# Optimization experiments

Hardware: AMD Instinct MI355X
Metric: run time of the kernel (lower is better)

## Reference

```python
import jax, jax.numpy as jnp
import numpy as np

N_NODES = 100000
N_EDGES = 1280000
IN_CH = 64
OUT_CH = 64


def setup_inputs() -> dict:
    key = jax.random.key(0)
    k1, k2, k3, k4 = jax.random.split(key, 4)
    x = jax.random.normal(k1, (N_NODES, IN_CH), dtype=jnp.float32)
    edge_index = jax.random.randint(k2, (2, N_EDGES), 0, N_NODES, dtype=jnp.int64)
    # GraphConv params (glorot weight, zero bias)
    scale = jnp.sqrt(6.0 / (IN_CH + OUT_CH)).astype(jnp.float32)
    W = jax.random.uniform(k3, (IN_CH, OUT_CH), dtype=jnp.float32, minval=-scale, maxval=scale)
    b = jnp.zeros((OUT_CH,), dtype=jnp.float32)
    return {"x": x, "edge_index": edge_index, "W": W, "b": b}


def reference(x, edge_index, W, b):
    # DGL GraphConv, norm='both': out = D_in^{-1/2} A^T (D_out^{-1/2} x W) + b
    src, dst = edge_index[0], edge_index[1]
    ones = jnp.ones((src.shape[0],), dtype=x.dtype)
    out_deg = jax.ops.segment_sum(ones, src, num_segments=N_NODES)
    in_deg = jax.ops.segment_sum(ones, dst, num_segments=N_NODES)
    norm_src = jnp.where(out_deg > 0, jax.lax.rsqrt(jnp.maximum(out_deg, 1.0)), 0.0)
    norm_dst = jnp.where(in_deg > 0, jax.lax.rsqrt(jnp.maximum(in_deg, 1.0)), 0.0)
    # in_feats <= out_feats: transform first, then aggregate
    h = (x * norm_src[:, None]) @ W              # [N, OUT_CH]
    msg = h[src]                                 # gather  [E, OUT_CH]
    agg = jax.ops.segment_sum(msg, dst, num_segments=N_NODES)  # scatter-add [N, OUT_CH]
    return agg * norm_dst[:, None] + b
```

## Files before the change

kernel.cpp:

```cpp
#include <hip/hip_runtime.h>
#include <hip/hip_fp16.h>

#define CH 64
#define CAP 32
#define SPILLMAX 4096
#define RANGE 12500
#define SLICES 64
#define TILE 2048
#define EPT 8
#define BSH 9
#define BKT 512

__global__ __launch_bounds__(256) void histA_kernel(const int* __restrict__ src,
                                                    const int* __restrict__ dst,
                                                    unsigned short* __restrict__ partial,
                                                    int* __restrict__ tileHist,
                                                    int* __restrict__ nspill,
                                                    int E, int N, int R, int NT)
{
    __shared__ int h[RANGE];
    int tid = threadIdx.x;
    int bid = blockIdx.x;
    if (bid < NT) {
        if (bid == 0 && tid == 0) nspill[0] = 0;
        h[tid] = 0;
        __syncthreads();
        int e0 = bid * TILE + tid * EPT;
        if (e0 + EPT <= E) {
            const int4* dp = (const int4*)(dst + e0);
            int4 a = dp[0], b = dp[1];
            atomicAdd(&h[a.x >> BSH], 1); atomicAdd(&h[a.y >> BSH], 1);
            atomicAdd(&h[a.z >> BSH], 1); atomicAdd(&h[a.w >> BSH], 1);
            atomicAdd(&h[b.x >> BSH], 1); atomicAdd(&h[b.y >> BSH], 1);
            atomicAdd(&h[b.z >> BSH], 1); atomicAdd(&h[b.w >> BSH], 1);
        } else {
            for (int k = e0; k < E && k < e0 + EPT; ++k) atomicAdd(&h[dst[k] >> BSH], 1);
        }
        __syncthreads();
        tileHist[bid * 256 + tid] = h[tid];
    } else {
        int hb = bid - NT;
        int r  = hb % R;
        int sl = hb / R;
        int lo = r * RANGE;
        int hi = min(lo + RANGE, N);
        int span = hi - lo;
        for (int i = tid; i < span; i += 256) h[i] = 0;
        __syncthreads();
        int per = (E + SLICES - 1) / SLICES;
        int sb = sl * per, se = min(sb + per, E);
        for (int e = sb + tid * 4; e < se; e += 256 * 4) {
            if (e + 4 <= se) {
                int4 v = *(const int4*)(src + e);
                if (v.x >= lo && v.x < hi) atomicAdd(&h[v.x - lo], 1);
                if (v.y >= lo && v.y < hi) atomicAdd(&h[v.y - lo], 1);
                if (v.z >= lo && v.z < hi) atomicAdd(&h[v.z - lo], 1);
                if (v.w >= lo && v.w < hi) atomicAdd(&h[v.w - lo], 1);
            } else {
                for (int k = e; k < se; ++k) {
                    int sv = src[k];
                    if (sv >= lo && sv < hi) atomicAdd(&h[sv - lo], 1);
                }
            }
        }
        __syncthreads();
        unsigned short* pp = partial + (size_t)hb * RANGE;
        for (int i = tid; i < span; i += 256) pp[i] = (unsigned short)h[i];
    }
}

__global__ __launch_bounds__(256) void rpscaleB_kernel(const unsigned short* __restrict__ partial,
                                                       const float* __restrict__ x,
                                                       __half* __restrict__ xh,
                                                       int* __restrict__ tileHist,
                                                       int* __restrict__ totals,
                                                       int N, int R, int NT, int NPB)
{
    __shared__ float nsl[256];
    __shared__ int sm[256];
    int tid = threadIdx.x;
    int bid = blockIdx.x;
    if (bid < NPB) {
        int n0 = bid * 256;
        int n = n0 + tid;
        if (n < N) {
            int r = n / RANGE, off = n - r * RANGE;
            int s = 0;
            #pragma unroll 8
            for (int sl = 0; sl < SLICES; ++sl)
                s += partial[(size_t)(sl * R + r) * RANGE + off];
            nsl[tid] = (s > 0) ? rsqrtf((float)s) : 0.0f;
        } else {
            nsl[tid] = 0.0f;
        }
        __syncthreads();
        int sub = tid & 7;
        int nl0 = tid >> 3;
        for (int p = 0; p < 8; ++p) {
            int nl = p * 32 + nl0;
            int node = n0 + nl;
            if (node >= N) break;
            float ns = nsl[nl];
            const float4* xp = (const float4*)(x + (size_t)node * CH + sub * 8);
            float4 a = xp[0], b = xp[1];
            __half2 h0 = __floats2half2_rn(a.x * ns, a.y * ns);
            __half2 h1 = __floats2half2_rn(a.z * ns, a.w * ns);
            __half2 h2 = __floats2half2_rn(b.x * ns, b.y * ns);
            __half2 h3 = __floats2half2_rn(b.z * ns, b.w * ns);
            uint4 u;
            u.x = (unsigned)__half_as_ushort(h0.x) | ((unsigned)__half_as_ushort(h0.y) << 16);
            u.y = (unsigned)__half_as_ushort(h1.x) | ((unsigned)__half_as_ushort(h1.y) << 16);
            u.z = (unsigned)__half_as_ushort(h2.x) | ((unsigned)__half_as_ushort(h2.y) << 16);
            u.w = (unsigned)__half_as_ushort(h3.x) | ((unsigned)__half_as_ushort(h3.y) << 16);
            *(uint4*)(xh + (size_t)node * CH + sub * 8) = u;
        }
    } else {
        int b = bid - NPB;
        int C = (NT + 255) / 256;
        int vals[8];
        int s = 0;
        for (int k = 0; k < C; ++k) {
            int t = tid * C + k;
            vals[k] = (t < NT) ? tileHist[t * 256 + b] : 0;
            s += vals[k];
        }
        sm[tid] = s;
        __syncthreads();
        for (int d = 1; d < 256; d <<= 1) {
            int v = (tid >= d) ? sm[tid - d] : 0;
            __syncthreads();
            sm[tid] += v;
            __syncthreads();
        }
        int off = (tid > 0) ? sm[tid - 1] : 0;
        for (int k = 0; k < C; ++k) {
            int t = tid * C + k;
            if (t < NT) { tileHist[t * 256 + b] = off; off += vals[k]; }
        }
        if (tid == 255) totals[b] = sm[255];
    }
}

__global__ __launch_bounds__(256) void binC_kernel(const int* __restrict__ src,
                                                   const int* __restrict__ dst,
                                                   const int* __restrict__ tileBase,
                                                   const int* __restrict__ totals,
                                                   int* __restrict__ sorted, int E, int NB)
{
    __shared__ int sm[256];
    __shared__ int gb[256];
    __shared__ int lcnt[256];
    __shared__ int lbase[256];
    __shared__ int slotVal[TILE];
    int tid = threadIdx.x;
    int t = blockIdx.x;
    sm[tid] = (tid < NB) ? totals[tid] : 0;
    lcnt[tid] = 0;
    __syncthreads();
    for (int d = 1; d < 256; d <<= 1) {
        int v = (tid >= d) ? sm[tid - d] : 0;
        __syncthreads();
        sm[tid] += v;
        __syncthreads();
    }
    int bb = (tid > 0) ? sm[tid - 1] : 0;
    gb[tid] = (tid < NB) ? bb + tileBase[t * 256 + tid] : 0;
    __syncthreads();
    int e0 = t * TILE + tid * EPT;
    int s[EPT], d[EPT], rk[EPT], pb[EPT];
    int nk = 0;
    if (e0 + EPT <= E) {
        const int4* sp = (const int4*)(src + e0);
        const int4* dp = (const int4*)(dst + e0);
        int4 a = sp[0], b = sp[1], c = dp[0], f = dp[1];
        s[0]=a.x; s[1]=a.y; s[2]=a.z; s[3]=a.w; s[4]=b.x; s[5]=b.y; s[6]=b.z; s[7]=b.w;
        d[0]=c.x; d[1]=c.y; d[2]=c.z; d[3]=c.w; d[4]=f.x; d[5]=f.y; d[6]=f.z; d[7]=f.w;
        nk = EPT;
    } else {
        for (int k = 0; e0 + k < E && k < EPT; ++k) { s[k] = src[e0+k]; d[k] = dst[e0+k]; nk++; }
    }
    for (int k = 0; k < nk; ++k) {
        pb[k] = d[k] >> BSH;
        rk[k] = atomicAdd(&lcnt[pb[k]], 1);
    }
    __syncthreads();
    sm[tid] = lcnt[tid];
    __syncthreads();
    for (int dd = 1; dd < 256; dd <<= 1) {
        int v = (tid >= dd) ? sm[tid - dd] : 0;
        __syncthreads();
        sm[tid] += v;
        __syncthreads();
    }
    lbase[tid] = (tid > 0) ? sm[tid - 1] : 0;
    int total = sm[255];
    __syncthreads();
    for (int k = 0; k < nk; ++k)
        slotVal[lbase[pb[k]] + rk[k]] = (s[k] << BSH) | (d[k] & (BKT - 1));
    __syncthreads();
    for (int i = tid; i < total; i += 256) {
        int lo = 0, hi = 255;
        #pragma unroll
        for (int st = 0; st < 8; ++st) {
            int mid = (lo + hi + 1) >> 1;
            if (lbase[mid] <= i) lo = mid; else hi = mid - 1;
        }
        sorted[gb[lo] + (i - lbase[lo])] = slotVal[i];
    }
}

__global__ __launch_bounds__(256) void binD_kernel(const int* __restrict__ sorted,
                                                   const int* __restrict__ totals,
                                                   int* __restrict__ bucket,
                                                   int* __restrict__ cnt,
                                                   int* __restrict__ spill,
                                                   int* __restrict__ nspill, int N, int NB)
{
    __shared__ int sm[256];
    __shared__ int lc[BKT];
    int b = blockIdx.x, tid = threadIdx.x;
    sm[tid] = (tid < NB) ? totals[tid] : 0;
    lc[tid] = 0; lc[tid + 256] = 0;
    __syncthreads();
    for (int d = 1; d < 256; d <<= 1) {
        int v = (tid >= d) ? sm[tid - d] : 0;
        __syncthreads();
        sm[tid] += v;
        __syncthreads();
    }
    int beg = (b > 0) ? sm[b - 1] : 0;
    int end = sm[b];
    int nbase = b << BSH;
    for (int i = beg + tid; i < end; i += 256) {
        int v = sorted[i];
        int sv = v >> BSH;
        int dl = v & (BKT - 1);
        int pos = atomicAdd(&lc[dl], 1);
        if (pos < CAP) {
            bucket[(size_t)(nbase + dl) * CAP + pos] = sv;
        } else {
            int sp = atomicAdd(nspill, 1);
            if (sp < SPILLMAX) { spill[2*sp] = nbase + dl; spill[2*sp+1] = sv; }
        }
    }
    __syncthreads();
    int n0 = nbase + tid;
    if (n0 < N) cnt[n0] = lc[tid];
    int n1 = nbase + 256 + tid;
    if (n1 < N) cnt[n1] = lc[256 + tid];
}

__global__ __launch_bounds__(256) void agg_kernel(const __half* __restrict__ xh,
                                                  const int* __restrict__ bucket,
                                                  const int* __restrict__ cnt,
                                                  const int* __restrict__ spill,
                                                  const int* __restrict__ nspill,
                                                  __half* __restrict__ aggh, int N)
{
    int hw0 = (blockIdx.x * blockDim.x + threadIdx.x) >> 5;
    int nHW = (gridDim.x * blockDim.x) >> 5;
    int sl = threadIdx.x & 31;
    for (int node = hw0; node < N; node += nHW) {
        int c = cnt[node];
        int m = (c < CAP) ? c : CAP;
        const int* bp = bucket + (size_t)node * CAP;
        float ax0 = 0, ay0 = 0, ax1 = 0, ay1 = 0, ax2 = 0, ay2 = 0, ax3 = 0, ay3 = 0;
        int j = 0;
        for (; j + 8 <= m; j += 8) {
            int4 va = *(const int4*)(bp + j);
            int4 vb = *(const int4*)(bp + j + 4);
            float2 f0 = __half22float2(*(const __half2*)(xh + (size_t)va.x * CH + sl * 2));
            float2 f1 = __half22float2(*(const __half2*)(xh + (size_t)va.y * CH + sl * 2));
            float2 f2 = __half22float2(*(const __half2*)(xh + (size_t)va.z * CH + sl * 2));
            float2 f3 = __half22float2(*(const __half2*)(xh + (size_t)va.w * CH + sl * 2));
            float2 f4 = __half22float2(*(const __half2*)(xh + (size_t)vb.x * CH + sl * 2));
            float2 f5 = __half22float2(*(const __half2*)(xh + (size_t)vb.y * CH + sl * 2));
            float2 f6 = __half22float2(*(const __half2*)(xh + (size_t)vb.z * CH + sl * 2));
            float2 f7 = __half22float2(*(const __half2*)(xh + (size_t)vb.w * CH + sl * 2));
            ax0 += f0.x + f4.x; ay0 += f0.y + f4.y;
            ax1 += f1.x + f5.x; ay1 += f1.y + f5.y;
            ax2 += f2.x + f6.x; ay2 += f2.y + f6.y;
            ax3 += f3.x + f7.x; ay3 += f3.y + f7.y;
        }
        for (; j + 4 <= m; j += 4) {
            int4 va = *(const int4*)(bp + j);
            float2 f0 = __half22float2(*(const __half2*)(xh + (size_t)va.x * CH + sl * 2));
            float2 f1 = __half22float2(*(const __half2*)(xh + (size_t)va.y * CH + sl * 2));
            float2 f2 = __half22float2(*(const __half2*)(xh + (size_t)va.z * CH + sl * 2));
            float2 f3 = __half22float2(*(const __half2*)(xh + (size_t)va.w * CH + sl * 2));
            ax0 += f0.x; ay0 += f0.y;
            ax1 += f1.x; ay1 += f1.y;
            ax2 += f2.x; ay2 += f2.y;
            ax3 += f3.x; ay3 += f3.y;
        }
        for (; j < m; ++j) {
            float2 f = __half22float2(*(const __half2*)(xh + (size_t)bp[j] * CH + sl * 2));
            ax0 += f.x; ay0 += f.y;
        }
        if (c > CAP) {
            int ns = *nspill;
            if (ns > SPILLMAX) ns = SPILLMAX;
            for (int i = 0; i < ns; ++i) {
                if (spill[2 * i] == node) {
                    float2 f = __half22float2(*(const __half2*)(xh + (size_t)spill[2 * i + 1] * CH + sl * 2));
                    ax0 += f.x; ay0 += f.y;
                }
            }
        }
        float nd = (c > 0) ? rsqrtf((float)c) : 0.0f;
        float rx = ((ax0 + ax1) + (ax2 + ax3)) * nd;
        float ry = ((ay0 + ay1) + (ay2 + ay3)) * nd;
        *(__half2*)(aggh + (size_t)node * CH + sl * 2) = __floats2half2_rn(rx, ry);
    }
}

__global__ __launch_bounds__(256) void gemm_out_kernel(const __half* __restrict__ aggh,
                                                       const float* __restrict__ W,
                                                       const float* __restrict__ bias,
                                                       float* __restrict__ out, int N)
{
    int g = blockIdx.x * 256 + threadIdx.x;
    int waveId = __builtin_amdgcn_readfirstlane(g >> 6);
    int lane = threadIdx.x & 63;
    int quarter = waveId & 3;
    int row = ((waveId >> 2) << 6) + lane;
    if (row >= N) return;
    const int cbase = quarter * 16;
    float acc[16];
    #pragma unroll
    for (int i = 0; i < 16; ++i) acc[i] = 0.0f;
    const __half* xp = aggh + (size_t)row * CH;
    for (int k0 = 0; k0 < CH; k0 += 8) {
        uint4 u = *(const uint4*)(xp + k0);
        const __half2* hp = (const __half2*)&u;
        float xk[8];
        #pragma unroll
        for (int j = 0; j < 4; ++j) {
            float2 f = __half22float2(hp[j]);
            xk[2 * j] = f.x; xk[2 * j + 1] = f.y;
        }
        #pragma unroll
        for (int kk = 0; kk < 8; ++kk) {
            const float* wrow = W + (k0 + kk) * CH + cbase;
            #pragma unroll
            for (int q = 0; q < 4; ++q) {
                float4 w = *(const float4*)(wrow + q * 4);
                acc[q * 4 + 0] += xk[kk] * w.x;
                acc[q * 4 + 1] += xk[kk] * w.y;
                acc[q * 4 + 2] += xk[kk] * w.z;
                acc[q * 4 + 3] += xk[kk] * w.w;
            }
        }
    }
    float* op = out + (size_t)row * CH + cbase;
    #pragma unroll
    for (int q = 0; q < 4; ++q) {
        float4 b = *(const float4*)(bias + cbase + q * 4);
        float4 o;
        o.x = acc[q * 4 + 0] + b.x;
        o.y = acc[q * 4 + 1] + b.y;
        o.z = acc[q * 4 + 2] + b.z;
        o.w = acc[q * 4 + 3] + b.w;
        *(float4*)(op + q * 4) = o;
    }
}

extern "C" void kernel_launch(void* const* d_in, const int* in_sizes, int n_in,
                              void* d_out, int out_size, void* d_ws, size_t ws_size,
                              hipStream_t stream)
{
    const float* x    = (const float*)d_in[0];
    const int*   edge = (const int*)d_in[1];
    const float* W    = (const float*)d_in[2];
    const float* bias = (const float*)d_in[3];
    float* out = (float*)d_out;

    int N = in_sizes[0] / CH;
    int E = in_sizes[1] / 2;
    const int* src = edge;
    const int* dst = edge + E;
    int R   = (N + RANGE - 1) / RANGE;
    int NT  = (E + TILE - 1) / TILE;
    int NB  = (N + BKT - 1) >> BSH;
    int NPB = (N + 255) / 256;

    int* nspill  = (int*)d_ws;
    int* spill   = nspill + 64;
    int* cnt     = spill + 2 * SPILLMAX;
    int* bucket  = cnt + N;
    unsigned short* partial = (unsigned short*)(bucket + (size_t)N * CAP);
    int* tileHist = (int*)(partial + (size_t)SLICES * R * RANGE);
    int* totals   = tileHist + NT * 256;
    int* sorted   = (int*)partial;
    size_t endoff = (char*)(totals + 320) - (char*)d_ws;
    size_t xoff = (endoff + 255) & ~(size_t)255;
    __half* xh = (__half*)((char*)d_ws + xoff);
    size_t aoff = ((xoff + (size_t)N * CH * sizeof(__half)) + 255) & ~(size_t)255;
    __half* aggh = (__half*)((char*)d_ws + aoff);

    histA_kernel<<<NT + R * SLICES, 256, 0, stream>>>(src, dst, partial, tileHist,
                                                      nspill, E, N, R, NT);
    rpscaleB_kernel<<<NPB + NB, 256, 0, stream>>>(partial, x, xh, tileHist, totals,
                                                  N, R, NT, NPB);
    binC_kernel<<<NT, 256, 0, stream>>>(src, dst, tileHist, totals, sorted, E, NB);
    binD_kernel<<<NB, 256, 0, stream>>>(sorted, totals, bucket, cnt, spill, nspill, N, NB);
    agg_kernel<<<4096, 256, 0, stream>>>(xh, bucket, cnt, spill, nspill, aggh, N);
    int nwaves = 4 * ((N + 63) / 64);
    gemm_out_kernel<<<(nwaves + 3) / 4, 256, 0, stream>>>(aggh, W, bias, out, N);
}
```

Baseline: 109.0 us.

## Pack out-degree histogram into 16-bit LDS counters and flatten agg grid

The out-degree histogram now packs two 16-bit counters per 32-bit LDS word, so each block covers 25000 nodes instead of 12500. That halves the range count R, while SLICES doubles to 128 to keep the block count. This halves the redundant source scans per slice, at the cost of shift/mask work and a reduction over twice as many partials in rpscaleB. The aggregation kernel also drops its grid-stride loop and launches one half-wave per node. Packed counters could overflow if a node got more than 65535 hits in one slice.

```diff
diff --git a/kernel.cpp b/kernel.cpp
--- a/kernel.cpp
+++ b/kernel.cpp
@@ -4,8 +4,9 @@
 #define CH 64
 #define CAP 32
 #define SPILLMAX 4096
-#define RANGE 12500
-#define SLICES 64
+#define HBINS 12500
+#define HSPAN 25000
+#define SLICES 128
 #define TILE 2048
 #define EPT 8
 #define BSH 9
@@ -13,12 +14,12 @@
 
 __global__ __launch_bounds__(256) void histA_kernel(const int* __restrict__ src,
                                                     const int* __restrict__ dst,
-                                                    unsigned short* __restrict__ partial,
+                                                    int* __restrict__ partial,
                                                     int* __restrict__ tileHist,
                                                     int* __restrict__ nspill,
                                                     int E, int N, int R, int NT)
 {
-    __shared__ int h[RANGE];
+    __shared__ int h[HBINS];
     int tid = threadIdx.x;
     int bid = blockIdx.x;
     if (bid < NT) {
@@ -42,34 +43,33 @@
         int hb = bid - NT;
         int r  = hb % R;
         int sl = hb / R;
-        int lo = r * RANGE;
-        int hi = min(lo + RANGE, N);
-        int span = hi - lo;
-        for (int i = tid; i < span; i += 256) h[i] = 0;
+        int lo = r * HSPAN;
+        int hi = min(lo + HSPAN, N);
+        for (int i = tid; i < HBINS; i += 256) h[i] = 0;
         __syncthreads();
         int per = (E + SLICES - 1) / SLICES;
         int sb = sl * per, se = min(sb + per, E);
         for (int e = sb + tid * 4; e < se; e += 256 * 4) {
             if (e + 4 <= se) {
                 int4 v = *(const int4*)(src + e);
-                if (v.x >= lo && v.x < hi) atomicAdd(&h[v.x - lo], 1);
-                if (v.y >= lo && v.y < hi) atomicAdd(&h[v.y - lo], 1);
-                if (v.z >= lo && v.z < hi) atomicAdd(&h[v.z - lo], 1);
-                if (v.w >= lo && v.w < hi) atomicAdd(&h[v.w - lo], 1);
+                if (v.x >= lo && v.x < hi) { int i0 = v.x - lo; atomicAdd(&h[i0 >> 1], 1u << ((i0 & 1) << 4)); }
+                if (v.y >= lo && v.y < hi) { int i1 = v.y - lo; atomicAdd(&h[i1 >> 1], 1u << ((i1 & 1) << 4)); }
+                if (v.z >= lo && v.z < hi) { int i2 = v.z - lo; atomicAdd(&h[i2 >> 1], 1u << ((i2 & 1) << 4)); }
+                if (v.w >= lo && v.w < hi) { int i3 = v.w - lo; atomicAdd(&h[i3 >> 1], 1u << ((i3 & 1) << 4)); }
             } else {
                 for (int k = e; k < se; ++k) {
                     int sv = src[k];
-                    if (sv >= lo && sv < hi) atomicAdd(&h[sv - lo], 1);
+                    if (sv >= lo && sv < hi) { int ii = sv - lo; atomicAdd(&h[ii >> 1], 1u << ((ii & 1) << 4)); }
                 }
             }
         }
         __syncthreads();
-        unsigned short* pp = partial + (size_t)hb * RANGE;
-        for (int i = tid; i < span; i += 256) pp[i] = (unsigned short)h[i];
-    }
-}
-
-__global__ __launch_bounds__(256) void rpscaleB_kernel(const unsigned short* __restrict__ partial,
+        int* pp = partial + (size_t)hb * HBINS;
+        for (int i = tid; i < HBINS; i += 256) pp[i] = h[i];
+    }
+}
+
+__global__ __launch_bounds__(256) void rpscaleB_kernel(const int* __restrict__ partial,
                                                        const float* __restrict__ x,
                                                        __half* __restrict__ xh,
                                                        int* __restrict__ tileHist,
@@ -84,11 +84,14 @@
         int n0 = bid * 256;
         int n = n0 + tid;
         if (n < N) {
-            int r = n / RANGE, off = n - r * RANGE;
+            int r = n / HSPAN;
+            int idx = n - r * HSPAN;
+            int word = idx >> 1;
+            int sh = (idx & 1) << 4;
             int s = 0;
             #pragma unroll 8
             for (int sl = 0; sl < SLICES; ++sl)
-                s += partial[(size_t)(sl * R + r) * RANGE + off];
+                s += (partial[(size_t)(sl * R + r) * HBINS + word] >> sh) & 0xFFFF;
             nsl[tid] = (s > 0) ? rsqrtf((float)s) : 0.0f;
         } else {
             nsl[tid] = 0.0f;
@@ -257,61 +260,59 @@
                                                   const int* __restrict__ nspill,
                                                   __half* __restrict__ aggh, int N)
 {
-    int hw0 = (blockIdx.x * blockDim.x + threadIdx.x) >> 5;
-    int nHW = (gridDim.x * blockDim.x) >> 5;
+    int node = (blockIdx.x * blockDim.x + threadIdx.x) >> 5;
     int sl = threadIdx.x & 31;
-    for (int node = hw0; node < N; node += nHW) {
-        int c = cnt[node];
-        int m = (c < CAP) ? c : CAP;
-        const int* bp = bucket + (size_t)node * CAP;
-        float ax0 = 0, ay0 = 0, ax1 = 0, ay1 = 0, ax2 = 0, ay2 = 0, ax3 = 0, ay3 = 0;
-        int j = 0;
-        for (; j + 8 <= m; j += 8) {
-            int4 va = *(const int4*)(bp + j);
-            int4 vb = *(const int4*)(bp + j + 4);
-            float2 f0 = __half22float2(*(const __half2*)(xh + (size_t)va.x * CH + sl * 2));
-            float2 f1 = __half22float2(*(const __half2*)(xh + (size_t)va.y * CH + sl * 2));
-            float2 f2 = __half22float2(*(const __half2*)(xh + (size_t)va.z * CH + sl * 2));
-            float2 f3 = __half22float2(*(const __half2*)(xh + (size_t)va.w * CH + sl * 2));
-            float2 f4 = __half22float2(*(const __half2*)(xh + (size_t)vb.x * CH + sl * 2));
-            float2 f5 = __half22float2(*(const __half2*)(xh + (size_t)vb.y * CH + sl * 2));
-            float2 f6 = __half22float2(*(const __half2*)(xh + (size_t)vb.z * CH + sl * 2));
-            float2 f7 = __half22float2(*(const __half2*)(xh + (size_t)vb.w * CH + sl * 2));
-            ax0 += f0.x + f4.x; ay0 += f0.y + f4.y;
-            ax1 += f1.x + f5.x; ay1 += f1.y + f5.y;
-            ax2 += f2.x + f6.x; ay2 += f2.y + f6.y;
-            ax3 += f3.x + f7.x; ay3 += f3.y + f7.y;
-        }
-        for (; j + 4 <= m; j += 4) {
-            int4 va = *(const int4*)(bp + j);
-            float2 f0 = __half22float2(*(const __half2*)(xh + (size_t)va.x * CH + sl * 2));
-            float2 f1 = __half22float2(*(const __half2*)(xh + (size_t)va.y * CH + sl * 2));
-            float2 f2 = __half22float2(*(const __half2*)(xh + (size_t)va.z * CH + sl * 2));
-            float2 f3 = __half22float2(*(const __half2*)(xh + (size_t)va.w * CH + sl * 2));
-            ax0 += f0.x; ay0 += f0.y;
-            ax1 += f1.x; ay1 += f1.y;
-            ax2 += f2.x; ay2 += f2.y;
-            ax3 += f3.x; ay3 += f3.y;
-        }
-        for (; j < m; ++j) {
-            float2 f = __half22float2(*(const __half2*)(xh + (size_t)bp[j] * CH + sl * 2));
-            ax0 += f.x; ay0 += f.y;
-        }
-        if (c > CAP) {
-            int ns = *nspill;
-            if (ns > SPILLMAX) ns = SPILLMAX;
-            for (int i = 0; i < ns; ++i) {
-                if (spill[2 * i] == node) {
-                    float2 f = __half22float2(*(const __half2*)(xh + (size_t)spill[2 * i + 1] * CH + sl * 2));
-                    ax0 += f.x; ay0 += f.y;
-                }
+    if (node >= N) return;
+    int c = cnt[node];
+    int m = (c < CAP) ? c : CAP;
+    const int* bp = bucket + (size_t)node * CAP;
+    float ax0 = 0, ay0 = 0, ax1 = 0, ay1 = 0, ax2 = 0, ay2 = 0, ax3 = 0, ay3 = 0;
+    int j = 0;
+    for (; j + 8 <= m; j += 8) {
+        int4 va = *(const int4*)(bp + j);
+        int4 vb = *(const int4*)(bp + j + 4);
+        float2 f0 = __half22float2(*(const __half2*)(xh + (size_t)va.x * CH + sl * 2));
+        float2 f1 = __half22float2(*(const __half2*)(xh + (size_t)va.y * CH + sl * 2));
+        float2 f2 = __half22float2(*(const __half2*)(xh + (size_t)va.z * CH + sl * 2));
+        float2 f3 = __half22float2(*(const __half2*)(xh + (size_t)va.w * CH + sl * 2));
+        float2 f4 = __half22float2(*(const __half2*)(xh + (size_t)vb.x * CH + sl * 2));
+        float2 f5 = __half22float2(*(const __half2*)(xh + (size_t)vb.y * CH + sl * 2));
+        float2 f6 = __half22float2(*(const __half2*)(xh + (size_t)vb.z * CH + sl * 2));
+        float2 f7 = __half22float2(*(const __half2*)(xh + (size_t)vb.w * CH + sl * 2));
+        ax0 += f0.x + f4.x; ay0 += f0.y + f4.y;
+        ax1 += f1.x + f5.x; ay1 += f1.y + f5.y;
+        ax2 += f2.x + f6.x; ay2 += f2.y + f6.y;
+        ax3 += f3.x + f7.x; ay3 += f3.y + f7.y;
+    }
+    for (; j + 4 <= m; j += 4) {
+        int4 va = *(const int4*)(bp + j);
+        float2 f0 = __half22float2(*(const __half2*)(xh + (size_t)va.x * CH + sl * 2));
+        float2 f1 = __half22float2(*(const __half2*)(xh + (size_t)va.y * CH + sl * 2));
+        float2 f2 = __half22float2(*(const __half2*)(xh + (size_t)va.z * CH + sl * 2));
+        float2 f3 = __half22float2(*(const __half2*)(xh + (size_t)va.w * CH + sl * 2));
+        ax0 += f0.x; ay0 += f0.y;
+        ax1 += f1.x; ay1 += f1.y;
+        ax2 += f2.x; ay2 += f2.y;
+        ax3 += f3.x; ay3 += f3.y;
+    }
+    for (; j < m; ++j) {
+        float2 f = __half22float2(*(const __half2*)(xh + (size_t)bp[j] * CH + sl * 2));
+        ax0 += f.x; ay0 += f.y;
+    }
+    if (c > CAP) {
+        int ns = *nspill;
+        if (ns > SPILLMAX) ns = SPILLMAX;
+        for (int i = 0; i < ns; ++i) {
+            if (spill[2 * i] == node) {
+                float2 f = __half22float2(*(const __half2*)(xh + (size_t)spill[2 * i + 1] * CH + sl * 2));
+                ax0 += f.x; ay0 += f.y;
             }
         }
-        float nd = (c > 0) ? rsqrtf((float)c) : 0.0f;
-        float rx = ((ax0 + ax1) + (ax2 + ax3)) * nd;
-        float ry = ((ay0 + ay1) + (ay2 + ay3)) * nd;
-        *(__half2*)(aggh + (size_t)node * CH + sl * 2) = __floats2half2_rn(rx, ry);
-    }
+    }
+    float nd = (c > 0) ? rsqrtf((float)c) : 0.0f;
+    float rx = ((ax0 + ax1) + (ax2 + ax3)) * nd;
+    float ry = ((ay0 + ay1) + (ay2 + ay3)) * nd;
+    *(__half2*)(aggh + (size_t)node * CH + sl * 2) = __floats2half2_rn(rx, ry);
 }
 
 __global__ __launch_bounds__(256) void gemm_out_kernel(const __half* __restrict__ aggh,
@@ -379,7 +380,7 @@
     int E = in_sizes[1] / 2;
     const int* src = edge;
     const int* dst = edge + E;
-    int R   = (N + RANGE - 1) / RANGE;
+    int R   = (N + HSPAN - 1) / HSPAN;
     int NT  = (E + TILE - 1) / TILE;
     int NB  = (N + BKT - 1) >> BSH;
     int NPB = (N + 255) / 256;
@@ -388,10 +389,10 @@
     int* spill   = nspill + 64;
     int* cnt     = spill + 2 * SPILLMAX;
     int* bucket  = cnt + N;
-    unsigned short* partial = (unsigned short*)(bucket + (size_t)N * CAP);
-    int* tileHist = (int*)(partial + (size_t)SLICES * R * RANGE);
+    int* partial = bucket + (size_t)N * CAP;
+    int* tileHist = partial + (size_t)R * SLICES * HBINS;
     int* totals   = tileHist + NT * 256;
-    int* sorted   = (int*)partial;
+    int* sorted   = partial;
     size_t endoff = (char*)(totals + 320) - (char*)d_ws;
     size_t xoff = (endoff + 255) & ~(size_t)255;
     __half* xh = (__half*)((char*)d_ws + xoff);
@@ -404,7 +405,8 @@
                                                   N, R, NT, NPB);
     binC_kernel<<<NT, 256, 0, stream>>>(src, dst, tileHist, totals, sorted, E, NB);
     binD_kernel<<<NB, 256, 0, stream>>>(sorted, totals, bucket, cnt, spill, nspill, N, NB);
-    agg_kernel<<<4096, 256, 0, stream>>>(xh, bucket, cnt, spill, nspill, aggh, N);
+    agg_kernel<<<((size_t)N * 32 + 255) / 256, 256, 0, stream>>>(xh, bucket, cnt, spill,
+                                                                 nspill, aggh, N);
     int nwaves = 4 * ((N + 63) / 64);
     gemm_out_kernel<<<(nwaves + 3) / 4, 256, 0, stream>>>(aggh, W, bias, out, N);
 }
```

Result: no change. 107.8 us, median of 2 (-1.1%).
